# Kernel optimization log

Hardware: AMD Instinct MI355X
Metric: run time of the kernel (lower is better)

## Reference

```python
import math
import jax, jax.numpy as jnp
import numpy as np

GROUPS = 32
EPS = 1e-5


def group_norm(x, w, b):
    # x: [B, C, H, W]
    B, C, H, W = x.shape
    xg = x.reshape(B, GROUPS, C // GROUPS, H, W)
    mean = xg.mean(axis=(2, 3, 4), keepdims=True)
    var = xg.var(axis=(2, 3, 4), keepdims=True)
    xg = (xg - mean) * jax.lax.rsqrt(var + EPS)
    x = xg.reshape(B, C, H, W)
    return x * w[None, :, None, None] + b[None, :, None, None]


def setup_inputs() -> dict:
    key = jax.random.key(0)
    ks = jax.random.split(key, 4)
    B, C, H, W = 16, 512, 32, 32
    x = jax.random.normal(ks[0], (B, C, H, W), dtype=jnp.float32)
    norm_w = jnp.ones((C,), dtype=jnp.float32)
    norm_b = jnp.zeros((C,), dtype=jnp.float32)
    qkv_w = jax.random.normal(ks[1], (3 * C, C), dtype=jnp.float32) / math.sqrt(C)
    qkv_b = jnp.zeros((3 * C,), dtype=jnp.float32)
    proj_w = jax.random.normal(ks[2], (C, C), dtype=jnp.float32) / math.sqrt(C)
    proj_b = jnp.zeros((C,), dtype=jnp.float32)
    return {"x": x, "norm_w": norm_w, "norm_b": norm_b,
            "qkv_w": qkv_w, "qkv_b": qkv_b,
            "proj_w": proj_w, "proj_b": proj_b}


def reference(x, norm_w, norm_b, qkv_w, qkv_b, proj_w, proj_b):
    B, C, H, W = x.shape
    xn = group_norm(x, norm_w, norm_b)
    # 1x1 conv == channel matmul: [B,3C,H,W]
    qkv = jnp.einsum('oc,bchw->bohw', qkv_w, xn) + qkv_b[None, :, None, None]
    q, k, v = jnp.split(qkv, 3, axis=1)
    q = q.reshape(B, C, H * W).transpose(0, 2, 1)  # [B, HW, C]
    k = k.reshape(B, C, H * W)                     # [B, C, HW]
    v = v.reshape(B, C, H * W).transpose(0, 2, 1)  # [B, HW, C]
    attn = jax.nn.softmax(jnp.einsum('bnc,bcm->bnm', q, k) / math.sqrt(C), axis=-1)
    h = jnp.einsum('bnm,bmc->bnc', attn, v)        # [B, HW, C]
    h = h.transpose(0, 2, 1).reshape(B, C, H, W)
    out = jnp.einsum('oc,bchw->bohw', proj_w, h) + proj_b[None, :, None, None]
    return out + x
```

## Files before the change

kernel.cpp:

```cpp
#include <hip/hip_runtime.h>

#define GLD16(gp, lp) __builtin_amdgcn_global_load_lds( \
    (const __attribute__((address_space(1))) void*)(gp), \
    (__attribute__((address_space(3))) void*)(lp), 16, 0, 0)

typedef __attribute__((ext_vector_type(8))) short bf16x8;
typedef __attribute__((ext_vector_type(4))) float f32x4;

__device__ __forceinline__ short f2bf(float f) {
    union { float f; unsigned u; } x; x.f = f;
    unsigned r = x.u + 0x7fffu + ((x.u >> 16) & 1u);
    return (short)(r >> 16);
}
__device__ __forceinline__ float bf2f(short s) {
    union { unsigned u; float f; } x;
    x.u = ((unsigned)(unsigned short)s) << 16;
    return x.f;
}

__global__ __launch_bounds__(256) void cvt_weights(
    const float* __restrict__ qkv_w, const float* __restrict__ proj_w,
    short* __restrict__ wq, short* __restrict__ wp)
{
    int idx = blockIdx.x * 256 + threadIdx.x;
    const int NQ4 = (1536 * 512) / 4;
    float4 f; short4 s;
    if (idx < NQ4) {
        f = ((const float4*)qkv_w)[idx];
        s.x = f2bf(f.x); s.y = f2bf(f.y); s.z = f2bf(f.z); s.w = f2bf(f.w);
        ((short4*)wq)[idx] = s;
    } else {
        int j = idx - NQ4;
        f = ((const float4*)proj_w)[j];
        s.x = f2bf(f.x); s.y = f2bf(f.y); s.z = f2bf(f.z); s.w = f2bf(f.w);
        ((short4*)wp)[j] = s;
    }
}

__global__ __launch_bounds__(256) void gn_stats(
    const float* __restrict__ x, float* __restrict__ mean, float* __restrict__ rstd)
{
    int bg = blockIdx.x;
    const float4* p = (const float4*)(x + (size_t)bg * 16384);
    float s = 0.f, ss = 0.f;
    for (int i = threadIdx.x; i < 4096; i += 256) {
        float4 v = p[i];
        s  += v.x + v.y + v.z + v.w;
        ss += v.x * v.x + v.y * v.y + v.z * v.z + v.w * v.w;
    }
    #pragma unroll
    for (int o = 32; o > 0; o >>= 1) {
        s  += __shfl_down(s, o);
        ss += __shfl_down(ss, o);
    }
    __shared__ float ls[4], lss[4];
    int wave = threadIdx.x >> 6;
    if ((threadIdx.x & 63) == 0) { ls[wave] = s; lss[wave] = ss; }
    __syncthreads();
    if (threadIdx.x == 0) {
        s  = ls[0] + ls[1] + ls[2] + ls[3];
        ss = lss[0] + lss[1] + lss[2] + lss[3];
        float m = s * (1.f / 16384.f);
        float var = ss * (1.f / 16384.f) - m * m;
        mean[bg] = m;
        rstd[bg] = rsqrtf(var + 1e-5f);
    }
}

__global__ __launch_bounds__(256) void gn_apply_t(
    const float* __restrict__ x, const float* __restrict__ w, const float* __restrict__ bb,
    const float* __restrict__ mean, const float* __restrict__ rstd,
    short* __restrict__ xnT)
{
    __shared__ short tile[64][65];
    int b = blockIdx.z, cblk = blockIdx.y, nblk = blockIdx.x;
    int t = threadIdx.x;
    int nl = t & 63;
    int cb = t >> 6;
    #pragma unroll
    for (int i = 0; i < 16; ++i) {
        int cl = cb * 16 + i;
        int cg = cblk * 64 + cl;
        int bgid = b * 32 + (cg >> 4);
        float sc = rstd[bgid] * w[cg];
        float sh = bb[cg] - mean[bgid] * sc;
        float xv = x[((size_t)(b * 512 + cg)) * 1024 + nblk * 64 + nl];
        tile[cl][nl] = f2bf(xv * sc + sh);
    }
    __syncthreads();
    int ng = t >> 4;
    int c4 = (t & 15) * 4;
    #pragma unroll
    for (int p = 0; p < 4; ++p) {
        int nl2 = p * 16 + ng;
        short4 sv;
        sv.x = tile[c4 + 0][nl2];
        sv.y = tile[c4 + 1][nl2];
        sv.z = tile[c4 + 2][nl2];
        sv.w = tile[c4 + 3][nl2];
        *(short4*)&xnT[((size_t)(b * 1024 + nblk * 64 + nl2)) * 512 + cblk * 64 + c4] = sv;
    }
}

__device__ __forceinline__ void gemm_nt_core(
    const short* __restrict__ A, const short* __restrict__ B,
    const int K, const int lda, const int ldb,
    short* lA, short* lB, f32x4 acc[4][4])
{
    const int t    = threadIdx.x;
    const int lane = t & 63;
    const int wave = t >> 6;
    const int wm = (wave >> 1) * 64;
    const int wn = (wave & 1) * 64;
    const int fr = lane & 15;
    const int fk = lane >> 4;
    const int arow = t >> 2;
    const int acol = (t & 3) * 8;

    const short* pa = A + (size_t)arow * lda + acol;
    const short* pb = B + (size_t)arow * ldb + acol;
    short* la_dst = lA + t * 8;
    short* lb_dst = lB + t * 8;
    const size_t astep = (size_t)64 * lda;
    const size_t bstep = (size_t)64 * ldb;

    for (int k0 = 0; k0 < K; k0 += 32) {
        GLD16(pa + k0,         la_dst);
        GLD16(pa + k0 + astep, la_dst + 2048);
        GLD16(pb + k0,         lb_dst);
        GLD16(pb + k0 + bstep, lb_dst + 2048);
        __syncthreads();
        bf16x8 af[4], bfr[4];
        #pragma unroll
        for (int m = 0; m < 4; ++m)
            af[m] = *(const bf16x8*)&lA[(wm + m * 16 + fr) * 32 + fk * 8];
        #pragma unroll
        for (int n = 0; n < 4; ++n)
            bfr[n] = *(const bf16x8*)&lB[(wn + n * 16 + fr) * 32 + fk * 8];
        #pragma unroll
        for (int m = 0; m < 4; ++m)
            #pragma unroll
            for (int n = 0; n < 4; ++n)
                acc[m][n] = __builtin_amdgcn_mfma_f32_16x16x32_bf16(af[m], bfr[n], acc[m][n], 0, 0, 0);
        __syncthreads();
    }
}

__global__ __launch_bounds__(256) void qkv_gemm(
    const short* __restrict__ wq, const float* __restrict__ qkv_b,
    const short* __restrict__ xnT,
    short* __restrict__ qT, short* __restrict__ kT, short* __restrict__ vv)
{
    __shared__ short lA[128 * 32], lB[128 * 32];
    const int b  = blockIdx.z;
    const int bm = blockIdx.y;
    const int bn = blockIdx.x;
    const short* A = wq + (size_t)bm * 128 * 512;
    const short* B = xnT + ((size_t)b * 1024 + bn * 128) * 512;
    f32x4 acc[4][4] = {};
    gemm_nt_core(A, B, 512, 512, 512, lA, lB, acc);

    const int lane = threadIdx.x & 63;
    const int wave = threadIdx.x >> 6;
    const int wm = (wave >> 1) * 64;
    const int wn = (wave & 1) * 64;
    const int fr = lane & 15;
    const int fk = lane >> 4;
    const int region = bm >> 2;
    const float qscale = 0.04419417382415922f;

    #pragma unroll
    for (int m = 0; m < 4; ++m) {
        int o0 = bm * 128 + wm + m * 16 + fk * 4;
        float4 bias = *(const float4*)&qkv_b[o0];
        #pragma unroll
        for (int n = 0; n < 4; ++n) {
            int col = bn * 128 + wn + n * 16 + fr;
            f32x4 a = acc[m][n];
            if (region == 0) {
                short4 sv;
                sv.x = f2bf((a[0] + bias.x) * qscale);
                sv.y = f2bf((a[1] + bias.y) * qscale);
                sv.z = f2bf((a[2] + bias.z) * qscale);
                sv.w = f2bf((a[3] + bias.w) * qscale);
                *(short4*)&qT[((size_t)(b * 1024 + col)) * 512 + o0] = sv;
            } else if (region == 1) {
                short4 sv;
                sv.x = f2bf(a[0] + bias.x);
                sv.y = f2bf(a[1] + bias.y);
                sv.z = f2bf(a[2] + bias.z);
                sv.w = f2bf(a[3] + bias.w);
                *(short4*)&kT[((size_t)(b * 1024 + col)) * 512 + (o0 - 512)] = sv;
            } else {
                float bb4[4] = {bias.x, bias.y, bias.z, bias.w};
                #pragma unroll
                for (int r = 0; r < 4; ++r)
                    vv[((size_t)(b * 512 + (o0 - 1024 + r))) * 1024 + col] = f2bf(a[r] + bb4[r]);
            }
        }
    }
}

__global__ __launch_bounds__(256) void s_gemm(
    const short* __restrict__ kT, const short* __restrict__ qT, short* __restrict__ S)
{
    __shared__ short lA[128 * 32], lB[128 * 32];
    const int b  = blockIdx.z;
    const int bm = blockIdx.y;
    const int bn = blockIdx.x;
    const short* A = kT + ((size_t)b * 1024 + bm * 128) * 512;
    const short* B = qT + ((size_t)b * 1024 + bn * 128) * 512;
    f32x4 acc[4][4] = {};
    gemm_nt_core(A, B, 512, 512, 512, lA, lB, acc);

    const int lane = threadIdx.x & 63;
    const int wave = threadIdx.x >> 6;
    const int wm = (wave >> 1) * 64;
    const int wn = (wave & 1) * 64;
    const int fr = lane & 15;
    const int fk = lane >> 4;

    #pragma unroll
    for (int m = 0; m < 4; ++m) {
        int m0 = bm * 128 + wm + m * 16 + fk * 4;
        #pragma unroll
        for (int n = 0; n < 4; ++n) {
            int ncol = bn * 128 + wn + n * 16 + fr;
            f32x4 a = acc[m][n];
            short4 sv;
            sv.x = f2bf(a[0]); sv.y = f2bf(a[1]); sv.z = f2bf(a[2]); sv.w = f2bf(a[3]);
            *(short4*)&S[((size_t)(b * 1024 + ncol)) * 1024 + m0] = sv;
        }
    }
}

__global__ __launch_bounds__(256) void softmax_rows(short* __restrict__ S)
{
    const int wave = threadIdx.x >> 6;
    const int lane = threadIdx.x & 63;
    size_t row = (size_t)blockIdx.x * 4 + wave;
    short* p = S + row * 1024;
    short4 raw[4];
    float v[16];
    #pragma unroll
    for (int i = 0; i < 4; ++i) raw[i] = ((short4*)p)[lane + 64 * i];
    #pragma unroll
    for (int i = 0; i < 4; ++i) {
        v[i * 4 + 0] = bf2f(raw[i].x);
        v[i * 4 + 1] = bf2f(raw[i].y);
        v[i * 4 + 2] = bf2f(raw[i].z);
        v[i * 4 + 3] = bf2f(raw[i].w);
    }
    float mx = v[0];
    #pragma unroll
    for (int i = 1; i < 16; ++i) mx = fmaxf(mx, v[i]);
    #pragma unroll
    for (int o = 1; o < 64; o <<= 1) mx = fmaxf(mx, __shfl_xor(mx, o));
    float sum = 0.f;
    #pragma unroll
    for (int i = 0; i < 16; ++i) { v[i] = __expf(v[i] - mx); sum += v[i]; }
    #pragma unroll
    for (int o = 1; o < 64; o <<= 1) sum += __shfl_xor(sum, o);
    float inv = 1.f / sum;
    #pragma unroll
    for (int i = 0; i < 4; ++i) {
        short4 sv;
        sv.x = f2bf(v[i * 4 + 0] * inv);
        sv.y = f2bf(v[i * 4 + 1] * inv);
        sv.z = f2bf(v[i * 4 + 2] * inv);
        sv.w = f2bf(v[i * 4 + 3] * inv);
        ((short4*)p)[lane + 64 * i] = sv;
    }
}

__global__ __launch_bounds__(256) void pv_gemm(
    const short* __restrict__ vv, const short* __restrict__ P, short* __restrict__ h)
{
    __shared__ short lA[128 * 32], lB[128 * 32];
    const int b  = blockIdx.z;
    const int bm = blockIdx.y;
    const int bn = blockIdx.x;
    const short* A = vv + ((size_t)b * 512 + bm * 128) * 1024;
    const short* B = P + ((size_t)b * 1024 + bn * 128) * 1024;
    f32x4 acc[4][4] = {};
    gemm_nt_core(A, B, 1024, 1024, 1024, lA, lB, acc);

    const int lane = threadIdx.x & 63;
    const int wave = threadIdx.x >> 6;
    const int wm = (wave >> 1) * 64;
    const int wn = (wave & 1) * 64;
    const int fr = lane & 15;
    const int fk = lane >> 4;

    #pragma unroll
    for (int m = 0; m < 4; ++m) {
        int c0 = bm * 128 + wm + m * 16 + fk * 4;
        #pragma unroll
        for (int n = 0; n < 4; ++n) {
            int ncol = bn * 128 + wn + n * 16 + fr;
            f32x4 a = acc[m][n];
            short4 sv;
            sv.x = f2bf(a[0]); sv.y = f2bf(a[1]); sv.z = f2bf(a[2]); sv.w = f2bf(a[3]);
            *(short4*)&h[((size_t)(b * 1024 + ncol)) * 512 + c0] = sv;
        }
    }
}

__global__ __launch_bounds__(256) void proj_gemm(
    const short* __restrict__ wp, const float* __restrict__ proj_b,
    const short* __restrict__ h, const float* __restrict__ x, float* __restrict__ out)
{
    __shared__ short lA[128 * 32], lB[128 * 32];
    const int b  = blockIdx.z;
    const int bm = blockIdx.y;
    const int bn = blockIdx.x;
    const short* A = wp + (size_t)bm * 128 * 512;
    const short* B = h + ((size_t)b * 1024 + bn * 128) * 512;
    f32x4 acc[4][4] = {};
    gemm_nt_core(A, B, 512, 512, 512, lA, lB, acc);

    const int lane = threadIdx.x & 63;
    const int wave = threadIdx.x >> 6;
    const int wm = (wave >> 1) * 64;
    const int wn = (wave & 1) * 64;
    const int fr = lane & 15;
    const int fk = lane >> 4;

    #pragma unroll
    for (int m = 0; m < 4; ++m) {
        int o0 = bm * 128 + wm + m * 16 + fk * 4;
        float4 pb = *(const float4*)&proj_b[o0];
        float pb4[4] = {pb.x, pb.y, pb.z, pb.w};
        #pragma unroll
        for (int n = 0; n < 4; ++n) {
            int col = bn * 128 + wn + n * 16 + fr;
            f32x4 a = acc[m][n];
            #pragma unroll
            for (int r = 0; r < 4; ++r) {
                size_t idx = ((size_t)(b * 512 + o0 + r)) * 1024 + col;
                out[idx] = a[r] + pb4[r] + x[idx];
            }
        }
    }
}

extern "C" void kernel_launch(void* const* d_in, const int* in_sizes, int n_in,
                              void* d_out, int out_size, void* d_ws, size_t ws_size,
                              hipStream_t stream) {
    const float* x      = (const float*)d_in[0];
    const float* norm_w = (const float*)d_in[1];
    const float* norm_b = (const float*)d_in[2];
    const float* qkv_w  = (const float*)d_in[3];
    const float* qkv_b  = (const float*)d_in[4];
    const float* proj_w = (const float*)d_in[5];
    const float* proj_b = (const float*)d_in[6];
    float* out = (float*)d_out;

    char* ws = (char*)d_ws;
    size_t off = 0;
    auto alloc = [&](size_t bytes) {
        void* p = ws + off;
        off = (off + bytes + 255) & ~(size_t)255;
        return p;
    };
    float* mean = (float*)alloc(512 * 4);
    float* rstd = (float*)alloc(512 * 4);
    short* wq   = (short*)alloc((size_t)1536 * 512 * 2);
    short* wp   = (short*)alloc((size_t)512 * 512 * 2);
    short* xnT  = (short*)alloc((size_t)16 * 1024 * 512 * 2);
    short* qT   = (short*)alloc((size_t)16 * 1024 * 512 * 2);
    short* kT   = (short*)alloc((size_t)16 * 1024 * 512 * 2);
    short* vv   = (short*)alloc((size_t)16 * 512 * 1024 * 2);
    short* S    = (short*)alloc((size_t)16 * 1024 * 1024 * 2);
    short* h    = xnT;

    cvt_weights<<<1024, 256, 0, stream>>>(qkv_w, proj_w, wq, wp);
    gn_stats<<<512, 256, 0, stream>>>(x, mean, rstd);
    gn_apply_t<<<dim3(16, 8, 16), 256, 0, stream>>>(x, norm_w, norm_b, mean, rstd, xnT);
    qkv_gemm<<<dim3(8, 12, 16), 256, 0, stream>>>(wq, qkv_b, xnT, qT, kT, vv);
    s_gemm<<<dim3(8, 8, 16), 256, 0, stream>>>(kT, qT, S);
    softmax_rows<<<4096, 256, 0, stream>>>(S);
    pv_gemm<<<dim3(8, 4, 16), 256, 0, stream>>>(vv, S, h);
    proj_gemm<<<dim3(8, 4, 16), 256, 0, stream>>>(wp, proj_b, h, x, out);
}
```

Baseline: 254.8 us.

## Rewrite GEMM core as 256x256 double-buffered tiles with swizzled LDS

```diff
diff --git a/kernel.cpp b/kernel.cpp
--- a/kernel.cpp
+++ b/kernel.cpp
@@ -102,97 +102,154 @@
     }
 }
 
-__device__ __forceinline__ void gemm_nt_core(
+__device__ __forceinline__ void gemm256(
     const short* __restrict__ A, const short* __restrict__ B,
-    const int K, const int lda, const int ldb,
-    short* lA, short* lB, f32x4 acc[4][4])
-{
-    const int t    = threadIdx.x;
-    const int lane = t & 63;
-    const int wave = t >> 6;
-    const int wm = (wave >> 1) * 64;
-    const int wn = (wave & 1) * 64;
+    const int lda, const int ldb, const int NT,
+    short* lds, f32x4 acc[8][4])
+{
+    const int tid  = threadIdx.x;
+    const int lane = tid & 63;
+    const int wave = tid >> 6;
+    const int wm = wave >> 2;
+    const int wn = wave & 3;
     const int fr = lane & 15;
     const int fk = lane >> 4;
-    const int arow = t >> 2;
-    const int acol = (t & 3) * 8;
-
-    const short* pa = A + (size_t)arow * lda + acol;
-    const short* pb = B + (size_t)arow * ldb + acol;
-    short* la_dst = lA + t * 8;
-    short* lb_dst = lB + t * 8;
-    const size_t astep = (size_t)64 * lda;
-    const size_t bstep = (size_t)64 * ldb;
-
-    for (int k0 = 0; k0 < K; k0 += 32) {
-        GLD16(pa + k0,         la_dst);
-        GLD16(pa + k0 + astep, la_dst + 2048);
-        GLD16(pb + k0,         lb_dst);
-        GLD16(pb + k0 + bstep, lb_dst + 2048);
-        __syncthreads();
-        bf16x8 af[4], bfr[4];
-        #pragma unroll
-        for (int m = 0; m < 4; ++m)
-            af[m] = *(const bf16x8*)&lA[(wm + m * 16 + fr) * 32 + fk * 8];
+    const int frx = fr & 7;
+
+    const short* pa[4]; const short* pb[4];
+    int la[4], lb[4];
+    #pragma unroll
+    for (int i = 0; i < 4; ++i) {
+        int cid = i * 512 + tid;
+        int row = cid >> 3;
+        int sl  = cid & 7;
+        int csw = sl ^ (row & 7);
+        pa[i] = A + (size_t)row * lda + csw * 8;
+        pb[i] = B + (size_t)row * ldb + csw * 8;
+        la[i] = cid * 8;
+        lb[i] = 16384 + cid * 8;
+    }
+
+    #pragma unroll
+    for (int i = 0; i < 4; ++i) GLD16(pa[i], lds + la[i]);
+    #pragma unroll
+    for (int i = 0; i < 4; ++i) GLD16(pb[i], lds + lb[i]);
+    #pragma unroll
+    for (int i = 0; i < 4; ++i) { pa[i] += 64; pb[i] += 64; }
+
+    const int arow0 = wm * 128 + fr;
+    const int brow0 = wn * 64 + fr;
+    const int slot0 = (fk ^ frx) << 3;
+    const int slot1 = ((4 + fk) ^ frx) << 3;
+
+    for (int t = 0; t < NT; ++t) {
+        const int cur = (t & 1) << 15;
+        const int nxt = 32768 - cur;
+        const bool pre = (t + 1 < NT);
+
+        if (pre) {
+            #pragma unroll
+            for (int i = 0; i < 4; ++i) GLD16(pa[i], lds + nxt + la[i]);
+        }
+        if (pre) asm volatile("s_waitcnt vmcnt(4)" ::: "memory");
+        else     asm volatile("s_waitcnt vmcnt(0)" ::: "memory");
+        asm volatile("s_barrier" ::: "memory");
+        __builtin_amdgcn_sched_barrier(0);
+
+        bf16x8 af[8], bfr[4];
+        #pragma unroll
+        for (int m = 0; m < 8; ++m)
+            af[m] = *(const bf16x8*)&lds[cur + ((arow0 + m * 16) << 6) + slot0];
         #pragma unroll
         for (int n = 0; n < 4; ++n)
-            bfr[n] = *(const bf16x8*)&lB[(wn + n * 16 + fr) * 32 + fk * 8];
-        #pragma unroll
-        for (int m = 0; m < 4; ++m)
+            bfr[n] = *(const bf16x8*)&lds[cur + 16384 + ((brow0 + n * 16) << 6) + slot0];
+        if (pre) {
+            #pragma unroll
+            for (int i = 0; i < 4; ++i) GLD16(pb[i], lds + nxt + lb[i]);
+        }
+        __builtin_amdgcn_s_setprio(1);
+        #pragma unroll
+        for (int m = 0; m < 8; ++m)
             #pragma unroll
             for (int n = 0; n < 4; ++n)
                 acc[m][n] = __builtin_amdgcn_mfma_f32_16x16x32_bf16(af[m], bfr[n], acc[m][n], 0, 0, 0);
-        __syncthreads();
-    }
-}
-
-__global__ __launch_bounds__(256) void qkv_gemm(
+        __builtin_amdgcn_s_setprio(0);
+
+        #pragma unroll
+        for (int m = 0; m < 8; ++m)
+            af[m] = *(const bf16x8*)&lds[cur + ((arow0 + m * 16) << 6) + slot1];
+        #pragma unroll
+        for (int n = 0; n < 4; ++n)
+            bfr[n] = *(const bf16x8*)&lds[cur + 16384 + ((brow0 + n * 16) << 6) + slot1];
+        __builtin_amdgcn_s_setprio(1);
+        #pragma unroll
+        for (int m = 0; m < 8; ++m)
+            #pragma unroll
+            for (int n = 0; n < 4; ++n)
+                acc[m][n] = __builtin_amdgcn_mfma_f32_16x16x32_bf16(af[m], bfr[n], acc[m][n], 0, 0, 0);
+        __builtin_amdgcn_s_setprio(0);
+
+        if (pre) {
+            #pragma unroll
+            for (int i = 0; i < 4; ++i) { pa[i] += 64; pb[i] += 64; }
+        }
+        asm volatile("s_barrier" ::: "memory");
+        __builtin_amdgcn_sched_barrier(0);
+    }
+}
+
+#define GEMM_EPI_IDX() \
+    const int lane = threadIdx.x & 63; \
+    const int wave = threadIdx.x >> 6; \
+    const int wm = wave >> 2; \
+    const int wn = wave & 3; \
+    const int fq = lane >> 4; \
+    const int fcol = lane & 15;
+
+__global__ __launch_bounds__(512, 2) void qkv_gemm(
     const short* __restrict__ wq, const float* __restrict__ qkv_b,
     const short* __restrict__ xnT,
     short* __restrict__ qT, short* __restrict__ kT, short* __restrict__ vv)
 {
-    __shared__ short lA[128 * 32], lB[128 * 32];
-    const int b  = blockIdx.z;
-    const int bm = blockIdx.y;
-    const int bn = blockIdx.x;
-    const short* A = wq + (size_t)bm * 128 * 512;
-    const short* B = xnT + ((size_t)b * 1024 + bn * 128) * 512;
-    f32x4 acc[4][4] = {};
-    gemm_nt_core(A, B, 512, 512, 512, lA, lB, acc);
-
-    const int lane = threadIdx.x & 63;
-    const int wave = threadIdx.x >> 6;
-    const int wm = (wave >> 1) * 64;
-    const int wn = (wave & 1) * 64;
-    const int fr = lane & 15;
-    const int fk = lane >> 4;
-    const int region = bm >> 2;
+    __shared__ short lds[65536];
+    const int b = blockIdx.z, bm = blockIdx.y, bn = blockIdx.x;
+    const short* A  = wq + (size_t)bm * 256 * 512;
+    const short* Bb = xnT + ((size_t)b * 1024 + bn * 256) * 512;
+    f32x4 acc[8][4];
+    #pragma unroll
+    for (int m = 0; m < 8; ++m)
+        #pragma unroll
+        for (int n = 0; n < 4; ++n) acc[m][n] = (f32x4){0.f, 0.f, 0.f, 0.f};
+    gemm256(A, Bb, 512, 512, 8, lds, acc);
+
+    GEMM_EPI_IDX();
+    const int region = bm >> 1;
     const float qscale = 0.04419417382415922f;
 
     #pragma unroll
-    for (int m = 0; m < 4; ++m) {
-        int o0 = bm * 128 + wm + m * 16 + fk * 4;
+    for (int m = 0; m < 8; ++m) {
+        int o0 = bm * 256 + wm * 128 + m * 16 + fq * 4;
         float4 bias = *(const float4*)&qkv_b[o0];
+        float bb4[4] = {bias.x, bias.y, bias.z, bias.w};
         #pragma unroll
         for (int n = 0; n < 4; ++n) {
-            int col = bn * 128 + wn + n * 16 + fr;
+            int col = bn * 256 + wn * 64 + n * 16 + fcol;
             f32x4 a = acc[m][n];
             if (region == 0) {
                 short4 sv;
-                sv.x = f2bf((a[0] + bias.x) * qscale);
-                sv.y = f2bf((a[1] + bias.y) * qscale);
-                sv.z = f2bf((a[2] + bias.z) * qscale);
-                sv.w = f2bf((a[3] + bias.w) * qscale);
+                sv.x = f2bf((a[0] + bb4[0]) * qscale);
+                sv.y = f2bf((a[1] + bb4[1]) * qscale);
+                sv.z = f2bf((a[2] + bb4[2]) * qscale);
+                sv.w = f2bf((a[3] + bb4[3]) * qscale);
                 *(short4*)&qT[((size_t)(b * 1024 + col)) * 512 + o0] = sv;
             } else if (region == 1) {
                 short4 sv;
-                sv.x = f2bf(a[0] + bias.x);
-                sv.y = f2bf(a[1] + bias.y);
-                sv.z = f2bf(a[2] + bias.z);
-                sv.w = f2bf(a[3] + bias.w);
+                sv.x = f2bf(a[0] + bb4[0]);
+                sv.y = f2bf(a[1] + bb4[1]);
+                sv.z = f2bf(a[2] + bb4[2]);
+                sv.w = f2bf(a[3] + bb4[3]);
                 *(short4*)&kT[((size_t)(b * 1024 + col)) * 512 + (o0 - 512)] = sv;
             } else {
-                float bb4[4] = {bias.x, bias.y, bias.z, bias.w};
                 #pragma unroll
                 for (int r = 0; r < 4; ++r)
                     vv[((size_t)(b * 512 + (o0 - 1024 + r))) * 1024 + col] = f2bf(a[r] + bb4[r]);
@@ -201,31 +258,27 @@
     }
 }
 
-__global__ __launch_bounds__(256) void s_gemm(
+__global__ __launch_bounds__(512, 2) void s_gemm(
     const short* __restrict__ kT, const short* __restrict__ qT, short* __restrict__ S)
 {
-    __shared__ short lA[128 * 32], lB[128 * 32];
-    const int b  = blockIdx.z;
-    const int bm = blockIdx.y;
-    const int bn = blockIdx.x;
-    const short* A = kT + ((size_t)b * 1024 + bm * 128) * 512;
-    const short* B = qT + ((size_t)b * 1024 + bn * 128) * 512;
-    f32x4 acc[4][4] = {};
-    gemm_nt_core(A, B, 512, 512, 512, lA, lB, acc);
-
-    const int lane = threadIdx.x & 63;
-    const int wave = threadIdx.x >> 6;
-    const int wm = (wave >> 1) * 64;
-    const int wn = (wave & 1) * 64;
-    const int fr = lane & 15;
-    const int fk = lane >> 4;
-
-    #pragma unroll
-    for (int m = 0; m < 4; ++m) {
-        int m0 = bm * 128 + wm + m * 16 + fk * 4;
+    __shared__ short lds[65536];
+    const int b = blockIdx.z, bm = blockIdx.y, bn = blockIdx.x;
+    const short* A  = kT + ((size_t)b * 1024 + bm * 256) * 512;
+    const short* Bb = qT + ((size_t)b * 1024 + bn * 256) * 512;
+    f32x4 acc[8][4];
+    #pragma unroll
+    for (int m = 0; m < 8; ++m)
+        #pragma unroll
+        for (int n = 0; n < 4; ++n) acc[m][n] = (f32x4){0.f, 0.f, 0.f, 0.f};
+    gemm256(A, Bb, 512, 512, 8, lds, acc);
+
+    GEMM_EPI_IDX();
+    #pragma unroll
+    for (int m = 0; m < 8; ++m) {
+        int m0 = bm * 256 + wm * 128 + m * 16 + fq * 4;
         #pragma unroll
         for (int n = 0; n < 4; ++n) {
-            int ncol = bn * 128 + wn + n * 16 + fr;
+            int ncol = bn * 256 + wn * 64 + n * 16 + fcol;
             f32x4 a = acc[m][n];
             short4 sv;
             sv.x = f2bf(a[0]); sv.y = f2bf(a[1]); sv.z = f2bf(a[2]); sv.w = f2bf(a[3]);
@@ -273,31 +326,27 @@
     }
 }
 
-__global__ __launch_bounds__(256) void pv_gemm(
+__global__ __launch_bounds__(512, 2) void pv_gemm(
     const short* __restrict__ vv, const short* __restrict__ P, short* __restrict__ h)
 {
-    __shared__ short lA[128 * 32], lB[128 * 32];
-    const int b  = blockIdx.z;
-    const int bm = blockIdx.y;
-    const int bn = blockIdx.x;
-    const short* A = vv + ((size_t)b * 512 + bm * 128) * 1024;
-    const short* B = P + ((size_t)b * 1024 + bn * 128) * 1024;
-    f32x4 acc[4][4] = {};
-    gemm_nt_core(A, B, 1024, 1024, 1024, lA, lB, acc);
-
-    const int lane = threadIdx.x & 63;
-    const int wave = threadIdx.x >> 6;
-    const int wm = (wave >> 1) * 64;
-    const int wn = (wave & 1) * 64;
-    const int fr = lane & 15;
-    const int fk = lane >> 4;
-
-    #pragma unroll
-    for (int m = 0; m < 4; ++m) {
-        int c0 = bm * 128 + wm + m * 16 + fk * 4;
+    __shared__ short lds[65536];
+    const int b = blockIdx.z, bm = blockIdx.y, bn = blockIdx.x;
+    const short* A  = vv + ((size_t)b * 512 + bm * 256) * 1024;
+    const short* Bb = P + ((size_t)b * 1024 + bn * 256) * 1024;
+    f32x4 acc[8][4];
+    #pragma unroll
+    for (int m = 0; m < 8; ++m)
+        #pragma unroll
+        for (int n = 0; n < 4; ++n) acc[m][n] = (f32x4){0.f, 0.f, 0.f, 0.f};
+    gemm256(A, Bb, 1024, 1024, 16, lds, acc);
+
+    GEMM_EPI_IDX();
+    #pragma unroll
+    for (int m = 0; m < 8; ++m) {
+        int c0 = bm * 256 + wm * 128 + m * 16 + fq * 4;
         #pragma unroll
         for (int n = 0; n < 4; ++n) {
-            int ncol = bn * 128 + wn + n * 16 + fr;
+            int ncol = bn * 256 + wn * 64 + n * 16 + fcol;
             f32x4 a = acc[m][n];
             short4 sv;
             sv.x = f2bf(a[0]); sv.y = f2bf(a[1]); sv.z = f2bf(a[2]); sv.w = f2bf(a[3]);
@@ -306,34 +355,30 @@
     }
 }
 
-__global__ __launch_bounds__(256) void proj_gemm(
+__global__ __launch_bounds__(512, 2) void proj_gemm(
     const short* __restrict__ wp, const float* __restrict__ proj_b,
     const short* __restrict__ h, const float* __restrict__ x, float* __restrict__ out)
 {
-    __shared__ short lA[128 * 32], lB[128 * 32];
-    const int b  = blockIdx.z;
-    const int bm = blockIdx.y;
-    const int bn = blockIdx.x;
-    const short* A = wp + (size_t)bm * 128 * 512;
-    const short* B = h + ((size_t)b * 1024 + bn * 128) * 512;
-    f32x4 acc[4][4] = {};
-    gemm_nt_core(A, B, 512, 512, 512, lA, lB, acc);
-
-    const int lane = threadIdx.x & 63;
-    const int wave = threadIdx.x >> 6;
-    const int wm = (wave >> 1) * 64;
-    const int wn = (wave & 1) * 64;
-    const int fr = lane & 15;
-    const int fk = lane >> 4;
-
-    #pragma unroll
-    for (int m = 0; m < 4; ++m) {
-        int o0 = bm * 128 + wm + m * 16 + fk * 4;
+    __shared__ short lds[65536];
+    const int b = blockIdx.z, bm = blockIdx.y, bn = blockIdx.x;
+    const short* A  = wp + (size_t)bm * 256 * 512;
+    const short* Bb = h + ((size_t)b * 1024 + bn * 256) * 512;
+    f32x4 acc[8][4];
+    #pragma unroll
+    for (int m = 0; m < 8; ++m)
+        #pragma unroll
+        for (int n = 0; n < 4; ++n) acc[m][n] = (f32x4){0.f, 0.f, 0.f, 0.f};
+    gemm256(A, Bb, 512, 512, 8, lds, acc);
+
+    GEMM_EPI_IDX();
+    #pragma unroll
+    for (int m = 0; m < 8; ++m) {
+        int o0 = bm * 256 + wm * 128 + m * 16 + fq * 4;
         float4 pb = *(const float4*)&proj_b[o0];
         float pb4[4] = {pb.x, pb.y, pb.z, pb.w};
         #pragma unroll
         for (int n = 0; n < 4; ++n) {
-            int col = bn * 128 + wn + n * 16 + fr;
+            int col = bn * 256 + wn * 64 + n * 16 + fcol;
             f32x4 a = acc[m][n];
             #pragma unroll
             for (int r = 0; r < 4; ++r) {
@@ -377,9 +422,9 @@
     cvt_weights<<<1024, 256, 0, stream>>>(qkv_w, proj_w, wq, wp);
     gn_stats<<<512, 256, 0, stream>>>(x, mean, rstd);
     gn_apply_t<<<dim3(16, 8, 16), 256, 0, stream>>>(x, norm_w, norm_b, mean, rstd, xnT);
-    qkv_gemm<<<dim3(8, 12, 16), 256, 0, stream>>>(wq, qkv_b, xnT, qT, kT, vv);
-    s_gemm<<<dim3(8, 8, 16), 256, 0, stream>>>(kT, qT, S);
+    qkv_gemm<<<dim3(4, 6, 16), 512, 0, stream>>>(wq, qkv_b, xnT, qT, kT, vv);
+    s_gemm<<<dim3(4, 4, 16), 512, 0, stream>>>(kT, qT, S);
     softmax_rows<<<4096, 256, 0, stream>>>(S);
-    pv_gemm<<<dim3(8, 4, 16), 256, 0, stream>>>(vv, S, h);
-    proj_gemm<<<dim3(8, 4, 16), 256, 0, stream>>>(wp, proj_b, h, x, out);
-}
+    pv_gemm<<<dim3(4, 2, 16), 512, 0, stream>>>(vv, S, h);
+    proj_gemm<<<dim3(4, 2, 16), 512, 0, stream>>>(wp, proj_b, h, x, out);
+}
```

Result: faster. 247.3 us (-2.9%).
